# Performance work log

Hardware: AMD Instinct MI355X
Metric: run time of the kernel (lower is better)

The kernel has to match this reference:

```python
import jax, jax.numpy as jnp
import numpy as np

N, E, C_IN, C_OUT = 50000, 800000, 64, 64
BN_EPS = 1e-5


def _batchnorm(h, gamma, beta):
    # Training-mode BatchNorm1d: batch statistics over dim 0, biased variance.
    mean = h.mean(axis=0)
    var = h.var(axis=0)  # ddof=0, matches PyTorch normalization stats
    return gamma * (h - mean) * jax.lax.rsqrt(var + BN_EPS) + beta


def setup_inputs() -> dict:
    key = jax.random.key(0)
    ks = jax.random.split(key, 6)
    x = jax.random.normal(ks[0], (N, C_IN), dtype=jnp.float32)
    edge_index = jax.random.randint(ks[1], (2, E), 0, N, dtype=jnp.int32)
    edge_weight = jax.random.uniform(ks[2], (E,), dtype=jnp.float32)
    s1 = 1.0 / np.sqrt(C_IN).astype(np.float32)
    s2 = 1.0 / np.sqrt(2 * C_IN).astype(np.float32)
    pool_W = jax.random.uniform(ks[3], (C_IN, C_IN), jnp.float32, -s1, s1)
    pool_b = jnp.zeros((C_IN,), jnp.float32)
    final_W = jax.random.uniform(ks[4], (2 * C_IN, C_OUT), jnp.float32, -s2, s2)
    final_b = jnp.zeros((C_OUT,), jnp.float32)
    return {
        "x": x,
        "edge_index": edge_index,
        "edge_weight": edge_weight,
        "pool_W": pool_W,
        "pool_b": pool_b,
        "bn_pool_gamma": jnp.ones((C_IN,), jnp.float32),
        "bn_pool_beta": jnp.zeros((C_IN,), jnp.float32),
        "final_W": final_W,
        "final_b": final_b,
        "bn_final_gamma": jnp.ones((C_OUT,), jnp.float32),
        "bn_final_beta": jnp.zeros((C_OUT,), jnp.float32),
        "coef": jnp.float32(0.5),
    }


def reference(x, edge_index, edge_weight, pool_W, pool_b, bn_pool_gamma,
              bn_pool_beta, final_W, final_b, bn_final_gamma, bn_final_beta,
              coef):
    src, dst = edge_index[0], edge_index[1]
    # gather src node features, scale by edge weight  -> [E, C_IN]
    edge_feat = x[src] * (1.0 + coef * edge_weight[:, None])
    pooled = edge_feat @ pool_W + pool_b              # [E, C_IN]
    pooled = jax.nn.relu(_batchnorm(pooled, bn_pool_gamma, bn_pool_beta))
    # scatter-max into destination nodes; empty segments -> 0 (pooled >= 0)
    agg = jax.ops.segment_max(pooled, dst, num_segments=x.shape[0])
    agg = jnp.maximum(agg, 0.0)                       # fill -inf (empty) with 0
    h = jnp.concatenate([x, agg], axis=-1) @ final_W + final_b  # [N, C_OUT]
    h = _batchnorm(h, bn_final_gamma, bn_final_beta)
    return jax.nn.relu(h)
```

## Files before the change

### kernel.cpp

```cpp
#include <hip/hip_runtime.h>
#include <hip/hip_fp16.h>
#include <math.h>
#include <float.h>

#define BN_EPS 1e-5f
#define SLOTS 64


typedef __attribute__((ext_vector_type(8))) short bf16x8;
typedef __attribute__((ext_vector_type(4))) float f32x4;

__device__ inline unsigned short f2bf(float f) {
    unsigned u = __float_as_uint(f);
    return (unsigned short)((u + 0x7fffu + ((u >> 16) & 1u)) >> 16);
}
__device__ inline float bf2f(unsigned short h) {
    return __uint_as_float(((unsigned)h) << 16);
}

__global__ __launch_bounds__(256, 4) void k_scatter_pool(
        const int* __restrict__ src, const int* __restrict__ dst,
        const float* __restrict__ w, const float* __restrict__ coef_p,
        int* __restrict__ cnt, unsigned* __restrict__ csr, int E,
        const float* __restrict__ x, const float* __restrict__ W,
        unsigned short* __restrict__ ybf, int nrows, int SB) {
    __shared__ unsigned short Wt[64 * 72];
    if ((int)blockIdx.x < SB) {
        const float coef = *coef_p;
        for (int i = blockIdx.x * 256 + threadIdx.x; i < E; i += SB * 256) {
            int tn = dst[i];
            int sn = src[i];
            float s = fmaf(coef, w[i], 1.0f);
            unsigned hs = (unsigned)__half_as_ushort(__float2half(s));
            int pos = atomicAdd(&cnt[tn], 1);
            if (pos < SLOTS)
                csr[(size_t)tn * SLOTS + pos] = ((unsigned)sn << 16) | hs;
        }
        return;
    }
    for (int i = threadIdx.x; i < 64 * 64; i += 256) {
        int k = i >> 6, n = i & 63;
        Wt[n * 72 + k] = f2bf(W[i]);
    }
    __syncthreads();
    const int lane = threadIdx.x & 63;
    const int wave = threadIdx.x >> 6;
    const int quad = lane >> 4;
    const int ln = lane & 15;
    bf16x8 Bf[2][4];
#pragma unroll
    for (int kc = 0; kc < 2; ++kc)
#pragma unroll
        for (int ct = 0; ct < 4; ++ct)
            Bf[kc][ct] = *(const bf16x8*)&Wt[(ct * 16 + ln) * 72 + kc * 32 + quad * 8];
    const int T = (nrows + 15) >> 4;
    const int gw = ((int)blockIdx.x - SB) * 4 + wave;
    const int nw = ((int)gridDim.x - SB) * 4;
    for (int t = gw; t < T; t += nw) {
        const int row = t * 16 + ln;
        bf16x8 af[2];
        if (row < nrows) {
            const float* xr = x + (size_t)row * 64;
#pragma unroll
            for (int kc = 0; kc < 2; ++kc) {
                float4 pv = *(const float4*)(xr + kc * 32 + quad * 8);
                float4 qv = *(const float4*)(xr + kc * 32 + quad * 8 + 4);
                bf16x8 a;
                a[0] = (short)f2bf(pv.x); a[1] = (short)f2bf(pv.y);
                a[2] = (short)f2bf(pv.z); a[3] = (short)f2bf(pv.w);
                a[4] = (short)f2bf(qv.x); a[5] = (short)f2bf(qv.y);
                a[6] = (short)f2bf(qv.z); a[7] = (short)f2bf(qv.w);
                af[kc] = a;
            }
        } else {
            bf16x8 z;
#pragma unroll
            for (int j = 0; j < 8; ++j) z[j] = 0;
            af[0] = z; af[1] = z;
        }
        f32x4 acc[4];
#pragma unroll
        for (int ct = 0; ct < 4; ++ct) { acc[ct][0]=0.f; acc[ct][1]=0.f; acc[ct][2]=0.f; acc[ct][3]=0.f; }
#pragma unroll
        for (int ct = 0; ct < 4; ++ct) {
            acc[ct] = __builtin_amdgcn_mfma_f32_16x16x32_bf16(af[0], Bf[0][ct], acc[ct], 0, 0, 0);
            acc[ct] = __builtin_amdgcn_mfma_f32_16x16x32_bf16(af[1], Bf[1][ct], acc[ct], 0, 0, 0);
        }
#pragma unroll
        for (int r = 0; r < 4; ++r) {
            int ro = t * 16 + quad * 4 + r;
            if (ro < nrows) {
#pragma unroll
                for (int ct = 0; ct < 4; ++ct)
                    ybf[(size_t)ro * 64 + ct * 16 + ln] = f2bf(acc[ct][r]);
            }
        }
    }
}

__global__ __launch_bounds__(256) void k_gather_max(const unsigned short* __restrict__ ybf,
                             const unsigned* __restrict__ csr, const int* __restrict__ cnt,
                             float* __restrict__ M, float* __restrict__ pG2, int nrows) {
    int sub = threadIdx.x & 15;
    int rg = threadIdx.x >> 4;
    int c0 = sub * 4;
    float s1[4] = {0, 0, 0, 0}, s2[4] = {0, 0, 0, 0};
    const int nchunks = (nrows + 15) >> 4;
    for (int nb = blockIdx.x; nb < nchunks; nb += gridDim.x) {
        int node = nb * 16 + rg;
        size_t base = (size_t)node * SLOTS;
        int dg = 0;
        if (node < nrows) { dg = cnt[node]; if (dg > SLOTS) dg = SLOTS; }
        float m0 = -FLT_MAX, m1 = -FLT_MAX, m2 = -FLT_MAX, m3 = -FLT_MAX;
        for (int k0 = 0; k0 < dg; k0 += 16) {
            int kk = k0 + sub;
            unsigned pk = (kk < dg) ? csr[base + kk] : 0u;
            int cnt16 = dg - k0; if (cnt16 > 16) cnt16 = 16;
            for (int j = 0; j < cnt16; ++j) {
                unsigned r = (unsigned)__shfl((int)pk, j, 16);
                int sn = r >> 16;
                float sv = __half2float(__ushort_as_half((unsigned short)(r & 0xffffu)));
                ushort4 uv = *(const ushort4*)&ybf[(size_t)sn * 64 + c0];
                float v0 = sv * bf2f(uv.x), v1 = sv * bf2f(uv.y);
                float v2 = sv * bf2f(uv.z), v3 = sv * bf2f(uv.w);
                m0 = fmaxf(m0, v0); s1[0] += v0; s2[0] = fmaf(v0, v0, s2[0]);
                m1 = fmaxf(m1, v1); s1[1] += v1; s2[1] = fmaf(v1, v1, s2[1]);
                m2 = fmaxf(m2, v2); s1[2] += v2; s2[2] = fmaf(v2, v2, s2[2]);
                m3 = fmaxf(m3, v3); s1[3] += v3; s2[3] = fmaf(v3, v3, s2[3]);
            }
        }
        if (node < nrows)
            *(float4*)&M[(size_t)node * 64 + c0] = make_float4(m0, m1, m2, m3);
    }
    __shared__ float red[16][68];
    float* prow = pG2 + (size_t)(blockIdx.x & 127) * 128;
#pragma unroll
    for (int j = 0; j < 4; ++j) red[rg][c0 + j] = s1[j];
    __syncthreads();
    if (rg == 0) {
#pragma unroll
        for (int j = 0; j < 4; ++j) {
            float tt = 0.0f;
            for (int r = 0; r < 16; ++r) tt += red[r][c0 + j];
            atomicAdd(&prow[c0 + j], tt);
        }
    }
    __syncthreads();
#pragma unroll
    for (int j = 0; j < 4; ++j) red[rg][c0 + j] = s2[j];
    __syncthreads();
    if (rg == 0) {
#pragma unroll
        for (int j = 0; j < 4; ++j) {
            float tt = 0.0f;
            for (int r = 0; r < 16; ++r) tt += red[r][c0 + j];
            atomicAdd(&prow[64 + c0 + j], tt);
        }
    }
}

__global__ __launch_bounds__(1024) void k_red2(const float* __restrict__ p2,
                             const float* __restrict__ pool_b, const float* __restrict__ gamma,
                             const float* __restrict__ beta, float invE,
                             float* __restrict__ coef) {
    int c = threadIdx.x & 127;
    int seg = threadIdx.x >> 7;
    float acc = 0.0f;
    for (int r = seg; r < 128; r += 8) acc += p2[(size_t)r * 128 + c];
    __shared__ float red[8][128];
    red[seg][c] = acc;
    __syncthreads();
    if (seg == 0) {
        float tt = 0.0f;
#pragma unroll
        for (int s = 0; s < 8; ++s) tt += red[s][c];
        red[0][c] = tt;
    }
    __syncthreads();
    if (threadIdx.x < 64) {
        int c0 = threadIdx.x;
        float S1 = red[0][c0], S2 = red[0][64 + c0];
        float s1 = S1 * invE;
        float b = pool_b[c0];
        float mean = s1 + b;
        float ex2 = S2 * invE + 2.0f * b * s1 + b * b;
        float var = ex2 - mean * mean;
        float a = gamma[c0] * rsqrtf(var + BN_EPS);
        coef[c0] = a;
        coef[64 + c0] = beta[c0] - a * s1;
    }
}

__global__ __launch_bounds__(1024) void k_red2f(const float* __restrict__ p2,
                             const float* __restrict__ gamma, const float* __restrict__ beta,
                             float invN, float* __restrict__ coef) {
    int c = threadIdx.x & 127;
    int seg = threadIdx.x >> 7;
    float acc = 0.0f;
    for (int r = seg; r < 128; r += 8) acc += p2[(size_t)r * 128 + c];
    __shared__ float red[8][128];
    red[seg][c] = acc;
    __syncthreads();
    if (seg == 0) {
        float tt = 0.0f;
#pragma unroll
        for (int s = 0; s < 8; ++s) tt += red[s][c];
        red[0][c] = tt;
    }
    __syncthreads();
    if (threadIdx.x < 64) {
        int c0 = threadIdx.x;
        float mean = red[0][c0] * invN;
        float var = red[0][64 + c0] * invN - mean * mean;
        float a = gamma[c0] * rsqrtf(var + BN_EPS);
        coef[c0] = a;
        coef[64 + c0] = beta[c0] - a * mean;
    }
}

__global__ __launch_bounds__(256, 2) void k_final_gemm(const float* __restrict__ x,
                             const float* __restrict__ M, const float* __restrict__ coef,
                             const float* __restrict__ W, const float* __restrict__ b,
                             float* __restrict__ h, float* __restrict__ pF2, int nrows) {
    __shared__ unsigned short Wt[64 * 136];
    __shared__ float hp[128];
    for (int i = threadIdx.x; i < 128 * 64; i += 256) {
        int k = i >> 6, n = i & 63;
        Wt[n * 136 + k] = f2bf(W[i]);
    }
    if (threadIdx.x < 128) hp[threadIdx.x] = 0.0f;
    __syncthreads();
    const int lane = threadIdx.x & 63;
    const int wave = threadIdx.x >> 6;
    const int quad = lane >> 4;
    const int ln = lane & 15;
    bf16x8 Bf[4][4];
#pragma unroll
    for (int kc = 0; kc < 4; ++kc)
#pragma unroll
        for (int ct = 0; ct < 4; ++ct)
            Bf[kc][ct] = *(const bf16x8*)&Wt[(ct * 16 + ln) * 136 + kc * 32 + quad * 8];
    float bias[4];
#pragma unroll
    for (int ct = 0; ct < 4; ++ct) bias[ct] = b[ct * 16 + ln];
    float ca[2][8], cd[2][8];
#pragma unroll
    for (int g = 0; g < 2; ++g) {
        int ch = g * 32 + quad * 8;
#pragma unroll
        for (int j = 0; j < 8; ++j) {
            ca[g][j] = coef[ch + j];
            cd[g][j] = coef[64 + ch + j];
        }
    }
    float ls1[4] = {0, 0, 0, 0}, ls2[4] = {0, 0, 0, 0};
    const int T = (nrows + 15) >> 4;
    const int gw = blockIdx.x * 4 + wave;
    const int nw = gridDim.x * 4;
    for (int t = gw; t < T; t += nw) {
        const int row = t * 16 + ln;
        bf16x8 af[4];
        if (row < nrows) {
            const float* xr = x + (size_t)row * 64;
#pragma unroll
            for (int kc = 0; kc < 2; ++kc) {
                float4 pv = *(const float4*)(xr + kc * 32 + quad * 8);
                float4 qv = *(const float4*)(xr + kc * 32 + quad * 8 + 4);
                bf16x8 a;
                a[0] = (short)f2bf(pv.x); a[1] = (short)f2bf(pv.y);
                a[2] = (short)f2bf(pv.z); a[3] = (short)f2bf(pv.w);
                a[4] = (short)f2bf(qv.x); a[5] = (short)f2bf(qv.y);
                a[6] = (short)f2bf(qv.z); a[7] = (short)f2bf(qv.w);
                af[kc] = a;
            }
            const float* mr = M + (size_t)row * 64;
#pragma unroll
            for (int g = 0; g < 2; ++g) {
                const float* mp = mr + g * 32 + quad * 8;
                float4 pv = *(const float4*)mp;
                float4 qv = *(const float4*)(mp + 4);
                float v[8] = {pv.x, pv.y, pv.z, pv.w, qv.x, qv.y, qv.z, qv.w};
                bf16x8 a;
#pragma unroll
                for (int j = 0; j < 8; ++j)
                    a[j] = (short)f2bf(fmaxf(fmaf(ca[g][j], v[j], cd[g][j]), 0.0f));
                af[2 + g] = a;
            }
        } else {
            bf16x8 z;
#pragma unroll
            for (int j = 0; j < 8; ++j) z[j] = 0;
#pragma unroll
            for (int kc = 0; kc < 4; ++kc) af[kc] = z;
        }
        f32x4 acc[4];
#pragma unroll
        for (int ct = 0; ct < 4; ++ct) { acc[ct][0]=0.f; acc[ct][1]=0.f; acc[ct][2]=0.f; acc[ct][3]=0.f; }
#pragma unroll
        for (int kc = 0; kc < 4; ++kc)
#pragma unroll
            for (int ct = 0; ct < 4; ++ct)
                acc[ct] = __builtin_amdgcn_mfma_f32_16x16x32_bf16(af[kc], Bf[kc][ct], acc[ct], 0, 0, 0);
#pragma unroll
        for (int r = 0; r < 4; ++r) {
            int ro = t * 16 + quad * 4 + r;
            if (ro < nrows) {
#pragma unroll
                for (int ct = 0; ct < 4; ++ct) {
                    float hv = acc[ct][r] + bias[ct];
                    h[(size_t)ro * 64 + ct * 16 + ln] = hv;
                    ls1[ct] += hv;
                    ls2[ct] = fmaf(hv, hv, ls2[ct]);
                }
            }
        }
    }
#pragma unroll
    for (int ct = 0; ct < 4; ++ct) {
        atomicAdd(&hp[ct * 16 + ln], ls1[ct]);
        atomicAdd(&hp[64 + ct * 16 + ln], ls2[ct]);
    }
    __syncthreads();
    if (threadIdx.x < 128)
        atomicAdd(&pF2[(size_t)(blockIdx.x & 127) * 128 + threadIdx.x], hp[threadIdx.x]);
}

__global__ __launch_bounds__(256) void k_bn_out(const float* __restrict__ h,
                         const float* __restrict__ coef,
                         float* __restrict__ out, int nrows) {
    const int idx = blockIdx.x * blockDim.x + threadIdx.x;
    const int total = nrows * 16;
    if (idx >= total) return;
    const int c0 = (idx & 15) * 4;
    const float4 hv = *(const float4*)(h + (size_t)idx * 4);
    float4 o;
    float* op = (float*)&o;
    const float* hp = (const float*)&hv;
#pragma unroll
    for (int j = 0; j < 4; ++j) {
        const int c = c0 + j;
        op[j] = fmaxf(fmaf(coef[c], hp[j], coef[64 + c]), 0.0f);
    }
    *(float4*)(out + (size_t)idx * 4) = o;
}

extern "C" void kernel_launch(void* const* d_in, const int* in_sizes, int n_in,
                              void* d_out, int out_size, void* d_ws, size_t ws_size,
                              hipStream_t stream) {
    const float* x       = (const float*)d_in[0];
    const int*   eidx    = (const int*)d_in[1];
    const float* ew      = (const float*)d_in[2];
    const float* pool_W  = (const float*)d_in[3];
    const float* pool_b  = (const float*)d_in[4];
    const float* g1      = (const float*)d_in[5];
    const float* b1      = (const float*)d_in[6];
    const float* final_W = (const float*)d_in[7];
    const float* final_b = (const float*)d_in[8];
    const float* g2      = (const float*)d_in[9];
    const float* b2      = (const float*)d_in[10];
    const float* coef    = (const float*)d_in[11];

    const int N = in_sizes[0] / 64;
    const int E = in_sizes[1] / 2;
    const int* src = eidx;
    const int* dst = eidx + E;

    const int SB  = 3072;
    const int T   = (N + 15) / 16;
    const int nbT = (T + 3) / 4;
    const int PG  = 1024;

    unsigned* ws = (unsigned*)d_ws;
    int*   cnt    = (int*)ws;
    float* pG2    = (float*)(ws + (size_t)N);
    float* pF2    = (float*)(ws + (size_t)N + 16384);
    float* bncoef = (float*)(ws + (size_t)N + 32768);
    float* coef2  = (float*)(ws + (size_t)N + 32896);
    unsigned short* ybf = (unsigned short*)(ws + (size_t)N + 33024);
    unsigned* csr = ws + (size_t)N + 33024 + (size_t)32 * N;
    float* M      = (float*)(csr + (size_t)SLOTS * N);

    hipMemsetAsync(d_ws, 0, ((size_t)N + 32768) * 4, stream);

    k_scatter_pool<<<SB + nbT, 256, 0, stream>>>(src, dst, ew, coef, cnt, csr, E,
                                                 x, pool_W, ybf, N, SB);
    k_gather_max<<<PG, 256, 0, stream>>>(ybf, csr, cnt, M, pG2, N);
    k_red2   <<<1, 1024, 0, stream>>>(pG2, pool_b, g1, b1, 1.0f / (float)E, bncoef);
    k_final_gemm<<<nbT, 256, 0, stream>>>(x, M, bncoef, final_W, final_b,
                                          (float*)d_out, pF2, N);
    k_red2f  <<<1, 1024, 0, stream>>>(pF2, g2, b2, 1.0f / (float)N, coef2);
    k_bn_out <<<(N * 16 + 255) / 256, 256, 0, stream>>>((const float*)d_out, coef2,
                                                        (float*)d_out, N);
}
```

Measured before the change: 221.9 us.

## Merge pipeline into one cooperative persistent kernel with grid barriers

Replaces the six separate launches (scatter+pool GEMM, gather-max, two BN reductions, final GEMM, BN output) with one persistent cooperative kernel that runs four phases separated by atomic grid barriers. The single-block BN statistic reductions are folded into the start of the next phase, with every block redundantly recomputing the coefficients. This removes launch gaps and tiny serial kernels. In exchange the grid is capped by occupancy (at most 1024 blocks), each phase uses fewer blocks than before, and the spin barriers plus host occupancy and device-property queries on every call add overhead.

```diff
diff --git a/kernel.cpp b/kernel.cpp
--- a/kernel.cpp
+++ b/kernel.cpp
@@ -18,330 +18,318 @@
     return __uint_as_float(((unsigned)h) << 16);
 }
 
-__global__ __launch_bounds__(256, 4) void k_scatter_pool(
+__device__ __forceinline__ void grid_bar(int* bcnt, int bar_idx) {
+    __syncthreads();
+    if (threadIdx.x == 0) {
+        __threadfence();
+        __hip_atomic_fetch_add(bcnt, 1, __ATOMIC_RELEASE, __HIP_MEMORY_SCOPE_AGENT);
+        const int target = (int)gridDim.x * bar_idx;
+        while (__hip_atomic_load(bcnt, __ATOMIC_RELAXED, __HIP_MEMORY_SCOPE_AGENT) < target)
+            __builtin_amdgcn_s_sleep(2);
+        __threadfence();
+    }
+    __syncthreads();
+}
+
+__global__ __launch_bounds__(256, 4) void k_mega(
         const int* __restrict__ src, const int* __restrict__ dst,
         const float* __restrict__ w, const float* __restrict__ coef_p,
-        int* __restrict__ cnt, unsigned* __restrict__ csr, int E,
-        const float* __restrict__ x, const float* __restrict__ W,
-        unsigned short* __restrict__ ybf, int nrows, int SB) {
-    __shared__ unsigned short Wt[64 * 72];
-    if ((int)blockIdx.x < SB) {
-        const float coef = *coef_p;
-        for (int i = blockIdx.x * 256 + threadIdx.x; i < E; i += SB * 256) {
-            int tn = dst[i];
-            int sn = src[i];
-            float s = fmaf(coef, w[i], 1.0f);
-            unsigned hs = (unsigned)__half_as_ushort(__float2half(s));
-            int pos = atomicAdd(&cnt[tn], 1);
-            if (pos < SLOTS)
-                csr[(size_t)tn * SLOTS + pos] = ((unsigned)sn << 16) | hs;
+        const float* __restrict__ x,
+        const float* __restrict__ pool_W, const float* __restrict__ pool_b,
+        const float* __restrict__ g1, const float* __restrict__ b1,
+        const float* __restrict__ final_W, const float* __restrict__ final_b,
+        const float* __restrict__ g2, const float* __restrict__ b2,
+        int* bcnt, int* __restrict__ cnt, unsigned* __restrict__ csr,
+        unsigned short* __restrict__ ybf, float* __restrict__ M,
+        float* __restrict__ pG2, float* __restrict__ pF2,
+        float* __restrict__ h, int N, int E, int SCB, int plo, int phi) {
+    __shared__ unsigned short Wt[64 * 136];
+    __shared__ float redf[16][68];
+    __shared__ float bnc[128];
+    __shared__ float hp[128];
+    const int tid = threadIdx.x;
+    const int bid = blockIdx.x;
+    const int nb  = gridDim.x;
+    const int lane = tid & 63;
+    const int wave = tid >> 6;
+    const int quad = lane >> 4;
+    const int ln   = lane & 15;
+    float* redflat = (float*)redf;
+
+    for (int ph = plo; ph <= phi; ++ph) {
+        switch (ph) {
+        case 0: {
+            if (bid < SCB) {
+                const float coef = *coef_p;
+                for (int i = bid * 256 + tid; i < E; i += SCB * 256) {
+                    int tn = dst[i];
+                    int sn = src[i];
+                    float s = fmaf(coef, w[i], 1.0f);
+                    unsigned hs = (unsigned)__half_as_ushort(__float2half(s));
+                    int pos = atomicAdd(&cnt[tn], 1);
+                    if (pos < SLOTS)
+                        csr[(size_t)tn * SLOTS + pos] = ((unsigned)sn << 16) | hs;
+                }
+            } else {
+                for (int i = tid; i < 64 * 64; i += 256) {
+                    int k = i >> 6, n = i & 63;
+                    Wt[n * 72 + k] = f2bf(pool_W[i]);
+                }
+                __syncthreads();
+                bf16x8 Bf[2][4];
+#pragma unroll
+                for (int kc = 0; kc < 2; ++kc)
+#pragma unroll
+                    for (int ct = 0; ct < 4; ++ct)
+                        Bf[kc][ct] = *(const bf16x8*)&Wt[(ct * 16 + ln) * 72 + kc * 32 + quad * 8];
+                const int T = (N + 15) >> 4;
+                const int gw = (bid - SCB) * 4 + wave;
+                const int nw = (nb - SCB) * 4;
+                for (int t = gw; t < T; t += nw) {
+                    const int row = t * 16 + ln;
+                    bf16x8 af[2];
+                    if (row < N) {
+                        const float* xr = x + (size_t)row * 64;
+#pragma unroll
+                        for (int kc = 0; kc < 2; ++kc) {
+                            float4 pv = *(const float4*)(xr + kc * 32 + quad * 8);
+                            float4 qv = *(const float4*)(xr + kc * 32 + quad * 8 + 4);
+                            bf16x8 a;
+                            a[0] = (short)f2bf(pv.x); a[1] = (short)f2bf(pv.y);
+                            a[2] = (short)f2bf(pv.z); a[3] = (short)f2bf(pv.w);
+                            a[4] = (short)f2bf(qv.x); a[5] = (short)f2bf(qv.y);
+                            a[6] = (short)f2bf(qv.z); a[7] = (short)f2bf(qv.w);
+                            af[kc] = a;
+                        }
+                    } else {
+                        bf16x8 z;
+#pragma unroll
+                        for (int j = 0; j < 8; ++j) z[j] = 0;
+                        af[0] = z; af[1] = z;
+                    }
+                    f32x4 acc[4];
+#pragma unroll
+                    for (int ct = 0; ct < 4; ++ct) { acc[ct][0]=0.f; acc[ct][1]=0.f; acc[ct][2]=0.f; acc[ct][3]=0.f; }
+#pragma unroll
+                    for (int ct = 0; ct < 4; ++ct) {
+                        acc[ct] = __builtin_amdgcn_mfma_f32_16x16x32_bf16(af[0], Bf[0][ct], acc[ct], 0, 0, 0);
+                        acc[ct] = __builtin_amdgcn_mfma_f32_16x16x32_bf16(af[1], Bf[1][ct], acc[ct], 0, 0, 0);
+                    }
+#pragma unroll
+                    for (int r = 0; r < 4; ++r) {
+                        int ro = t * 16 + quad * 4 + r;
+                        if (ro < N) {
+#pragma unroll
+                            for (int ct = 0; ct < 4; ++ct)
+                                ybf[(size_t)ro * 64 + ct * 16 + ln] = f2bf(acc[ct][r]);
+                        }
+                    }
+                }
+            }
+            break;
         }
-        return;
+        case 1: {
+            int sub = tid & 15;
+            int rg = tid >> 4;
+            int c0 = sub * 4;
+            float s1[4] = {0, 0, 0, 0}, s2[4] = {0, 0, 0, 0};
+            const int nchunks = (N + 15) >> 4;
+            for (int nbk = bid; nbk < nchunks; nbk += nb) {
+                int node = nbk * 16 + rg;
+                size_t base = (size_t)node * SLOTS;
+                int dg = 0;
+                if (node < N) { dg = cnt[node]; if (dg > SLOTS) dg = SLOTS; }
+                float m0 = -FLT_MAX, m1 = -FLT_MAX, m2 = -FLT_MAX, m3 = -FLT_MAX;
+                for (int k0 = 0; k0 < dg; k0 += 16) {
+                    int kk = k0 + sub;
+                    unsigned pk = (kk < dg) ? csr[base + kk] : 0u;
+                    int cnt16 = dg - k0; if (cnt16 > 16) cnt16 = 16;
+                    for (int j = 0; j < cnt16; ++j) {
+                        unsigned r = (unsigned)__shfl((int)pk, j, 16);
+                        int sn = r >> 16;
+                        float sv = __half2float(__ushort_as_half((unsigned short)(r & 0xffffu)));
+                        ushort4 uv = *(const ushort4*)&ybf[(size_t)sn * 64 + c0];
+                        float v0 = sv * bf2f(uv.x), v1 = sv * bf2f(uv.y);
+                        float v2 = sv * bf2f(uv.z), v3 = sv * bf2f(uv.w);
+                        m0 = fmaxf(m0, v0); s1[0] += v0; s2[0] = fmaf(v0, v0, s2[0]);
+                        m1 = fmaxf(m1, v1); s1[1] += v1; s2[1] = fmaf(v1, v1, s2[1]);
+                        m2 = fmaxf(m2, v2); s1[2] += v2; s2[2] = fmaf(v2, v2, s2[2]);
+                        m3 = fmaxf(m3, v3); s1[3] += v3; s2[3] = fmaf(v3, v3, s2[3]);
+                    }
+                }
+                if (node < N)
+                    *(float4*)&M[(size_t)node * 64 + c0] = make_float4(m0, m1, m2, m3);
+            }
+            float* prow = pG2 + (size_t)(bid & 127) * 128;
+            __syncthreads();
+#pragma unroll
+            for (int j = 0; j < 4; ++j) redf[rg][c0 + j] = s1[j];
+            __syncthreads();
+            if (rg == 0) {
+#pragma unroll
+                for (int j = 0; j < 4; ++j) {
+                    float tt = 0.0f;
+                    for (int r = 0; r < 16; ++r) tt += redf[r][c0 + j];
+                    atomicAdd(&prow[c0 + j], tt);
+                }
+            }
+            __syncthreads();
+#pragma unroll
+            for (int j = 0; j < 4; ++j) redf[rg][c0 + j] = s2[j];
+            __syncthreads();
+            if (rg == 0) {
+#pragma unroll
+                for (int j = 0; j < 4; ++j) {
+                    float tt = 0.0f;
+                    for (int r = 0; r < 16; ++r) tt += redf[r][c0 + j];
+                    atomicAdd(&prow[64 + c0 + j], tt);
+                }
+            }
+            break;
+        }
+        case 2: {
+            for (int i = tid; i < 128 * 64; i += 256) {
+                int k = i >> 6, n = i & 63;
+                Wt[n * 136 + k] = f2bf(final_W[i]);
+            }
+            int c = tid & 127, seg = tid >> 7;
+            float acc = 0.0f;
+            for (int r = seg; r < 128; r += 2) acc += pG2[(size_t)r * 128 + c];
+            __syncthreads();
+            redflat[tid] = acc;
+            __syncthreads();
+            if (tid < 64) {
+                float S1 = redflat[tid] + redflat[128 + tid];
+                float S2 = redflat[64 + tid] + redflat[192 + tid];
+                float invE = 1.0f / (float)E;
+                float s1m = S1 * invE;
+                float bb = pool_b[tid];
+                float mean = s1m + bb;
+                float ex2 = S2 * invE + 2.0f * bb * s1m + bb * bb;
+                float var = ex2 - mean * mean;
+                float a = g1[tid] * rsqrtf(var + BN_EPS);
+                bnc[tid] = a;
+                bnc[64 + tid] = b1[tid] - a * s1m;
+            }
+            if (tid < 128) hp[tid] = 0.0f;
+            __syncthreads();
+
+            bf16x8 Bf[4][4];
+#pragma unroll
+            for (int kc = 0; kc < 4; ++kc)
+#pragma unroll
+                for (int ct = 0; ct < 4; ++ct)
+                    Bf[kc][ct] = *(const bf16x8*)&Wt[(ct * 16 + ln) * 136 + kc * 32 + quad * 8];
+            float bias[4];
+#pragma unroll
+            for (int ct = 0; ct < 4; ++ct) bias[ct] = final_b[ct * 16 + ln];
+            float ls1[4] = {0, 0, 0, 0}, ls2[4] = {0, 0, 0, 0};
+            const int T = (N + 15) >> 4;
+            const int gw = bid * 4 + wave;
+            const int nw = nb * 4;
+            for (int t = gw; t < T; t += nw) {
+                const int row = t * 16 + ln;
+                bf16x8 af[4];
+                if (row < N) {
+                    const float* xr = x + (size_t)row * 64;
+#pragma unroll
+                    for (int kc = 0; kc < 2; ++kc) {
+                        float4 pv = *(const float4*)(xr + kc * 32 + quad * 8);
+                        float4 qv = *(const float4*)(xr + kc * 32 + quad * 8 + 4);
+                        bf16x8 a;
+                        a[0] = (short)f2bf(pv.x); a[1] = (short)f2bf(pv.y);
+                        a[2] = (short)f2bf(pv.z); a[3] = (short)f2bf(pv.w);
+                        a[4] = (short)f2bf(qv.x); a[5] = (short)f2bf(qv.y);
+                        a[6] = (short)f2bf(qv.z); a[7] = (short)f2bf(qv.w);
+                        af[kc] = a;
+                    }
+                    const float* mr = M + (size_t)row * 64;
+#pragma unroll
+                    for (int g = 0; g < 2; ++g) {
+                        const float* mp = mr + g * 32 + quad * 8;
+                        float4 pv = *(const float4*)mp;
+                        float4 qv = *(const float4*)(mp + 4);
+                        float v[8] = {pv.x, pv.y, pv.z, pv.w, qv.x, qv.y, qv.z, qv.w};
+                        int ch = g * 32 + quad * 8;
+                        bf16x8 a;
+#pragma unroll
+                        for (int j = 0; j < 8; ++j)
+                            a[j] = (short)f2bf(fmaxf(fmaf(bnc[ch + j], v[j], bnc[64 + ch + j]), 0.0f));
+                        af[2 + g] = a;
+                    }
+                } else {
+                    bf16x8 z;
+#pragma unroll
+                    for (int j = 0; j < 8; ++j) z[j] = 0;
+#pragma unroll
+                    for (int kc = 0; kc < 4; ++kc) af[kc] = z;
+                }
+                f32x4 acc4[4];
+#pragma unroll
+                for (int ct = 0; ct < 4; ++ct) { acc4[ct][0]=0.f; acc4[ct][1]=0.f; acc4[ct][2]=0.f; acc4[ct][3]=0.f; }
+#pragma unroll
+                for (int kc = 0; kc < 4; ++kc)
+#pragma unroll
+                    for (int ct = 0; ct < 4; ++ct)
+                        acc4[ct] = __builtin_amdgcn_mfma_f32_16x16x32_bf16(af[kc], Bf[kc][ct], acc4[ct], 0, 0, 0);
+#pragma unroll
+                for (int r = 0; r < 4; ++r) {
+                    int ro = t * 16 + quad * 4 + r;
+                    if (ro < N) {
+#pragma unroll
+                        for (int ct = 0; ct < 4; ++ct) {
+                            float hv = acc4[ct][r] + bias[ct];
+                            h[(size_t)ro * 64 + ct * 16 + ln] = hv;
+                            ls1[ct] += hv;
+                            ls2[ct] = fmaf(hv, hv, ls2[ct]);
+                        }
+                    }
+                }
+            }
+#pragma unroll
+            for (int ct = 0; ct < 4; ++ct) {
+                atomicAdd(&hp[ct * 16 + ln], ls1[ct]);
+                atomicAdd(&hp[64 + ct * 16 + ln], ls2[ct]);
+            }
+            __syncthreads();
+            if (tid < 128)
+                atomicAdd(&pF2[(size_t)(bid & 127) * 128 + tid], hp[tid]);
+            break;
+        }
+        case 3: {
+            int c = tid & 127, seg = tid >> 7;
+            float acc = 0.0f;
+            for (int r = seg; r < 128; r += 2) acc += pF2[(size_t)r * 128 + c];
+            __syncthreads();
+            redflat[tid] = acc;
+            __syncthreads();
+            if (tid < 64) {
+                float S1 = redflat[tid] + redflat[128 + tid];
+                float S2 = redflat[64 + tid] + redflat[192 + tid];
+                float invN = 1.0f / (float)N;
+                float mean = S1 * invN;
+                float var = S2 * invN - mean * mean;
+                float a = g2[tid] * rsqrtf(var + BN_EPS);
+                bnc[tid] = a;
+                bnc[64 + tid] = b2[tid] - a * mean;
+            }
+            __syncthreads();
+            const int total = N * 16;
+            for (int idx = bid * 256 + tid; idx < total; idx += nb * 256) {
+                const int c0 = (idx & 15) * 4;
+                float4 hv = *(const float4*)(h + (size_t)idx * 4);
+                float4 o;
+                o.x = fmaxf(fmaf(bnc[c0 + 0], hv.x, bnc[64 + c0 + 0]), 0.0f);
+                o.y = fmaxf(fmaf(bnc[c0 + 1], hv.y, bnc[64 + c0 + 1]), 0.0f);
+                o.z = fmaxf(fmaf(bnc[c0 + 2], hv.z, bnc[64 + c0 + 2]), 0.0f);
+                o.w = fmaxf(fmaf(bnc[c0 + 3], hv.w, bnc[64 + c0 + 3]), 0.0f);
+                *(float4*)(h + (size_t)idx * 4) = o;
+            }
+            break;
+        }
+        }
+        if (ph < phi) grid_bar(bcnt, ph - plo + 1);
     }
-    for (int i = threadIdx.x; i < 64 * 64; i += 256) {
-        int k = i >> 6, n = i & 63;
-        Wt[n * 72 + k] = f2bf(W[i]);
-    }
-    __syncthreads();
-    const int lane = threadIdx.x & 63;
-    const int wave = threadIdx.x >> 6;
-    const int quad = lane >> 4;
-    const int ln = lane & 15;
-    bf16x8 Bf[2][4];
-#pragma unroll
-    for (int kc = 0; kc < 2; ++kc)
-#pragma unroll
-        for (int ct = 0; ct < 4; ++ct)
-            Bf[kc][ct] = *(const bf16x8*)&Wt[(ct * 16 + ln) * 72 + kc * 32 + quad * 8];
-    const int T = (nrows + 15) >> 4;
-    const int gw = ((int)blockIdx.x - SB) * 4 + wave;
-    const int nw = ((int)gridDim.x - SB) * 4;
-    for (int t = gw; t < T; t += nw) {
-        const int row = t * 16 + ln;
-        bf16x8 af[2];
-        if (row < nrows) {
-            const float* xr = x + (size_t)row * 64;
-#pragma unroll
-            for (int kc = 0; kc < 2; ++kc) {
-                float4 pv = *(const float4*)(xr + kc * 32 + quad * 8);
-                float4 qv = *(const float4*)(xr + kc * 32 + quad * 8 + 4);
-                bf16x8 a;
-                a[0] = (short)f2bf(pv.x); a[1] = (short)f2bf(pv.y);
-                a[2] = (short)f2bf(pv.z); a[3] = (short)f2bf(pv.w);
-                a[4] = (short)f2bf(qv.x); a[5] = (short)f2bf(qv.y);
-                a[6] = (short)f2bf(qv.z); a[7] = (short)f2bf(qv.w);
-                af[kc] = a;
-            }
-        } else {
-            bf16x8 z;
-#pragma unroll
-            for (int j = 0; j < 8; ++j) z[j] = 0;
-            af[0] = z; af[1] = z;
-        }
-        f32x4 acc[4];
-#pragma unroll
-        for (int ct = 0; ct < 4; ++ct) { acc[ct][0]=0.f; acc[ct][1]=0.f; acc[ct][2]=0.f; acc[ct][3]=0.f; }
-#pragma unroll
-        for (int ct = 0; ct < 4; ++ct) {
-            acc[ct] = __builtin_amdgcn_mfma_f32_16x16x32_bf16(af[0], Bf[0][ct], acc[ct], 0, 0, 0);
-            acc[ct] = __builtin_amdgcn_mfma_f32_16x16x32_bf16(af[1], Bf[1][ct], acc[ct], 0, 0, 0);
-        }
-#pragma unroll
-        for (int r = 0; r < 4; ++r) {
-            int ro = t * 16 + quad * 4 + r;
-            if (ro < nrows) {
-#pragma unroll
-                for (int ct = 0; ct < 4; ++ct)
-                    ybf[(size_t)ro * 64 + ct * 16 + ln] = f2bf(acc[ct][r]);
-            }
-        }
-    }
-}
-
-__global__ __launch_bounds__(256) void k_gather_max(const unsigned short* __restrict__ ybf,
-                             const unsigned* __restrict__ csr, const int* __restrict__ cnt,
-                             float* __restrict__ M, float* __restrict__ pG2, int nrows) {
-    int sub = threadIdx.x & 15;
-    int rg = threadIdx.x >> 4;
-    int c0 = sub * 4;
-    float s1[4] = {0, 0, 0, 0}, s2[4] = {0, 0, 0, 0};
-    const int nchunks = (nrows + 15) >> 4;
-    for (int nb = blockIdx.x; nb < nchunks; nb += gridDim.x) {
-        int node = nb * 16 + rg;
-        size_t base = (size_t)node * SLOTS;
-        int dg = 0;
-        if (node < nrows) { dg = cnt[node]; if (dg > SLOTS) dg = SLOTS; }
-        float m0 = -FLT_MAX, m1 = -FLT_MAX, m2 = -FLT_MAX, m3 = -FLT_MAX;
-        for (int k0 = 0; k0 < dg; k0 += 16) {
-            int kk = k0 + sub;
-            unsigned pk = (kk < dg) ? csr[base + kk] : 0u;
-            int cnt16 = dg - k0; if (cnt16 > 16) cnt16 = 16;
-            for (int j = 0; j < cnt16; ++j) {
-                unsigned r = (unsigned)__shfl((int)pk, j, 16);
-                int sn = r >> 16;
-                float sv = __half2float(__ushort_as_half((unsigned short)(r & 0xffffu)));
-                ushort4 uv = *(const ushort4*)&ybf[(size_t)sn * 64 + c0];
-                float v0 = sv * bf2f(uv.x), v1 = sv * bf2f(uv.y);
-                float v2 = sv * bf2f(uv.z), v3 = sv * bf2f(uv.w);
-                m0 = fmaxf(m0, v0); s1[0] += v0; s2[0] = fmaf(v0, v0, s2[0]);
-                m1 = fmaxf(m1, v1); s1[1] += v1; s2[1] = fmaf(v1, v1, s2[1]);
-                m2 = fmaxf(m2, v2); s1[2] += v2; s2[2] = fmaf(v2, v2, s2[2]);
-                m3 = fmaxf(m3, v3); s1[3] += v3; s2[3] = fmaf(v3, v3, s2[3]);
-            }
-        }
-        if (node < nrows)
-            *(float4*)&M[(size_t)node * 64 + c0] = make_float4(m0, m1, m2, m3);
-    }
-    __shared__ float red[16][68];
-    float* prow = pG2 + (size_t)(blockIdx.x & 127) * 128;
-#pragma unroll
-    for (int j = 0; j < 4; ++j) red[rg][c0 + j] = s1[j];
-    __syncthreads();
-    if (rg == 0) {
-#pragma unroll
-        for (int j = 0; j < 4; ++j) {
-            float tt = 0.0f;
-            for (int r = 0; r < 16; ++r) tt += red[r][c0 + j];
-            atomicAdd(&prow[c0 + j], tt);
-        }
-    }
-    __syncthreads();
-#pragma unroll
-    for (int j = 0; j < 4; ++j) red[rg][c0 + j] = s2[j];
-    __syncthreads();
-    if (rg == 0) {
-#pragma unroll
-        for (int j = 0; j < 4; ++j) {
-            float tt = 0.0f;
-            for (int r = 0; r < 16; ++r) tt += red[r][c0 + j];
-            atomicAdd(&prow[64 + c0 + j], tt);
-        }
-    }
-}
-
-__global__ __launch_bounds__(1024) void k_red2(const float* __restrict__ p2,
-                             const float* __restrict__ pool_b, const float* __restrict__ gamma,
-                             const float* __restrict__ beta, float invE,
-                             float* __restrict__ coef) {
-    int c = threadIdx.x & 127;
-    int seg = threadIdx.x >> 7;
-    float acc = 0.0f;
-    for (int r = seg; r < 128; r += 8) acc += p2[(size_t)r * 128 + c];
-    __shared__ float red[8][128];
-    red[seg][c] = acc;
-    __syncthreads();
-    if (seg == 0) {
-        float tt = 0.0f;
-#pragma unroll
-        for (int s = 0; s < 8; ++s) tt += red[s][c];
-        red[0][c] = tt;
-    }
-    __syncthreads();
-    if (threadIdx.x < 64) {
-        int c0 = threadIdx.x;
-        float S1 = red[0][c0], S2 = red[0][64 + c0];
-        float s1 = S1 * invE;
-        float b = pool_b[c0];
-        float mean = s1 + b;
-        float ex2 = S2 * invE + 2.0f * b * s1 + b * b;
-        float var = ex2 - mean * mean;
-        float a = gamma[c0] * rsqrtf(var + BN_EPS);
-        coef[c0] = a;
-        coef[64 + c0] = beta[c0] - a * s1;
-    }
-}
-
-__global__ __launch_bounds__(1024) void k_red2f(const float* __restrict__ p2,
-                             const float* __restrict__ gamma, const float* __restrict__ beta,
-                             float invN, float* __restrict__ coef) {
-    int c = threadIdx.x & 127;
-    int seg = threadIdx.x >> 7;
-    float acc = 0.0f;
-    for (int r = seg; r < 128; r += 8) acc += p2[(size_t)r * 128 + c];
-    __shared__ float red[8][128];
-    red[seg][c] = acc;
-    __syncthreads();
-    if (seg == 0) {
-        float tt = 0.0f;
-#pragma unroll
-        for (int s = 0; s < 8; ++s) tt += red[s][c];
-        red[0][c] = tt;
-    }
-    __syncthreads();
-    if (threadIdx.x < 64) {
-        int c0 = threadIdx.x;
-        float mean = red[0][c0] * invN;
-        float var = red[0][64 + c0] * invN - mean * mean;
-        float a = gamma[c0] * rsqrtf(var + BN_EPS);
-        coef[c0] = a;
-        coef[64 + c0] = beta[c0] - a * mean;
-    }
-}
-
-__global__ __launch_bounds__(256, 2) void k_final_gemm(const float* __restrict__ x,
-                             const float* __restrict__ M, const float* __restrict__ coef,
-                             const float* __restrict__ W, const float* __restrict__ b,
-                             float* __restrict__ h, float* __restrict__ pF2, int nrows) {
-    __shared__ unsigned short Wt[64 * 136];
-    __shared__ float hp[128];
-    for (int i = threadIdx.x; i < 128 * 64; i += 256) {
-        int k = i >> 6, n = i & 63;
-        Wt[n * 136 + k] = f2bf(W[i]);
-    }
-    if (threadIdx.x < 128) hp[threadIdx.x] = 0.0f;
-    __syncthreads();
-    const int lane = threadIdx.x & 63;
-    const int wave = threadIdx.x >> 6;
-    const int quad = lane >> 4;
-    const int ln = lane & 15;
-    bf16x8 Bf[4][4];
-#pragma unroll
-    for (int kc = 0; kc < 4; ++kc)
-#pragma unroll
-        for (int ct = 0; ct < 4; ++ct)
-            Bf[kc][ct] = *(const bf16x8*)&Wt[(ct * 16 + ln) * 136 + kc * 32 + quad * 8];
-    float bias[4];
-#pragma unroll
-    for (int ct = 0; ct < 4; ++ct) bias[ct] = b[ct * 16 + ln];
-    float ca[2][8], cd[2][8];
-#pragma unroll
-    for (int g = 0; g < 2; ++g) {
-        int ch = g * 32 + quad * 8;
-#pragma unroll
-        for (int j = 0; j < 8; ++j) {
-            ca[g][j] = coef[ch + j];
-            cd[g][j] = coef[64 + ch + j];
-        }
-    }
-    float ls1[4] = {0, 0, 0, 0}, ls2[4] = {0, 0, 0, 0};
-    const int T = (nrows + 15) >> 4;
-    const int gw = blockIdx.x * 4 + wave;
-    const int nw = gridDim.x * 4;
-    for (int t = gw; t < T; t += nw) {
-        const int row = t * 16 + ln;
-        bf16x8 af[4];
-        if (row < nrows) {
-            const float* xr = x + (size_t)row * 64;
-#pragma unroll
-            for (int kc = 0; kc < 2; ++kc) {
-                float4 pv = *(const float4*)(xr + kc * 32 + quad * 8);
-                float4 qv = *(const float4*)(xr + kc * 32 + quad * 8 + 4);
-                bf16x8 a;
-                a[0] = (short)f2bf(pv.x); a[1] = (short)f2bf(pv.y);
-                a[2] = (short)f2bf(pv.z); a[3] = (short)f2bf(pv.w);
-                a[4] = (short)f2bf(qv.x); a[5] = (short)f2bf(qv.y);
-                a[6] = (short)f2bf(qv.z); a[7] = (short)f2bf(qv.w);
-                af[kc] = a;
-            }
-            const float* mr = M + (size_t)row * 64;
-#pragma unroll
-            for (int g = 0; g < 2; ++g) {
-                const float* mp = mr + g * 32 + quad * 8;
-                float4 pv = *(const float4*)mp;
-                float4 qv = *(const float4*)(mp + 4);
-                float v[8] = {pv.x, pv.y, pv.z, pv.w, qv.x, qv.y, qv.z, qv.w};
-                bf16x8 a;
-#pragma unroll
-                for (int j = 0; j < 8; ++j)
-                    a[j] = (short)f2bf(fmaxf(fmaf(ca[g][j], v[j], cd[g][j]), 0.0f));
-                af[2 + g] = a;
-            }
-        } else {
-            bf16x8 z;
-#pragma unroll
-            for (int j = 0; j < 8; ++j) z[j] = 0;
-#pragma unroll
-            for (int kc = 0; kc < 4; ++kc) af[kc] = z;
-        }
-        f32x4 acc[4];
-#pragma unroll
-        for (int ct = 0; ct < 4; ++ct) { acc[ct][0]=0.f; acc[ct][1]=0.f; acc[ct][2]=0.f; acc[ct][3]=0.f; }
-#pragma unroll
-        for (int kc = 0; kc < 4; ++kc)
-#pragma unroll
-            for (int ct = 0; ct < 4; ++ct)
-                acc[ct] = __builtin_amdgcn_mfma_f32_16x16x32_bf16(af[kc], Bf[kc][ct], acc[ct], 0, 0, 0);
-#pragma unroll
-        for (int r = 0; r < 4; ++r) {
-            int ro = t * 16 + quad * 4 + r;
-            if (ro < nrows) {
-#pragma unroll
-                for (int ct = 0; ct < 4; ++ct) {
-                    float hv = acc[ct][r] + bias[ct];
-                    h[(size_t)ro * 64 + ct * 16 + ln] = hv;
-                    ls1[ct] += hv;
-                    ls2[ct] = fmaf(hv, hv, ls2[ct]);
-                }
-            }
-        }
-    }
-#pragma unroll
-    for (int ct = 0; ct < 4; ++ct) {
-        atomicAdd(&hp[ct * 16 + ln], ls1[ct]);
-        atomicAdd(&hp[64 + ct * 16 + ln], ls2[ct]);
-    }
-    __syncthreads();
-    if (threadIdx.x < 128)
-        atomicAdd(&pF2[(size_t)(blockIdx.x & 127) * 128 + threadIdx.x], hp[threadIdx.x]);
-}
-
-__global__ __launch_bounds__(256) void k_bn_out(const float* __restrict__ h,
-                         const float* __restrict__ coef,
-                         float* __restrict__ out, int nrows) {
-    const int idx = blockIdx.x * blockDim.x + threadIdx.x;
-    const int total = nrows * 16;
-    if (idx >= total) return;
-    const int c0 = (idx & 15) * 4;
-    const float4 hv = *(const float4*)(h + (size_t)idx * 4);
-    float4 o;
-    float* op = (float*)&o;
-    const float* hp = (const float*)&hv;
-#pragma unroll
-    for (int j = 0; j < 4; ++j) {
-        const int c = c0 + j;
-        op[j] = fmaxf(fmaf(coef[c], hp[j], coef[64 + c]), 0.0f);
-    }
-    *(float4*)(out + (size_t)idx * 4) = o;
 }
 
 extern "C" void kernel_launch(void* const* d_in, const int* in_sizes, int n_in,
@@ -360,35 +348,69 @@
     const float* b2      = (const float*)d_in[10];
     const float* coef    = (const float*)d_in[11];
 
-    const int N = in_sizes[0] / 64;
-    const int E = in_sizes[1] / 2;
+    int N = in_sizes[0] / 64;
+    int E = in_sizes[1] / 2;
     const int* src = eidx;
     const int* dst = eidx + E;
 
-    const int SB  = 3072;
-    const int T   = (N + 15) / 16;
-    const int nbT = (T + 3) / 4;
-    const int PG  = 1024;
-
     unsigned* ws = (unsigned*)d_ws;
-    int*   cnt    = (int*)ws;
-    float* pG2    = (float*)(ws + (size_t)N);
-    float* pF2    = (float*)(ws + (size_t)N + 16384);
-    float* bncoef = (float*)(ws + (size_t)N + 32768);
-    float* coef2  = (float*)(ws + (size_t)N + 32896);
-    unsigned short* ybf = (unsigned short*)(ws + (size_t)N + 33024);
-    unsigned* csr = ws + (size_t)N + 33024 + (size_t)32 * N;
+    int*   bcnt  = (int*)ws;
+    int*   cnt   = (int*)(ws + 2);
+    float* pG2   = (float*)(ws + 2 + (size_t)N);
+    float* pF2   = (float*)(ws + 2 + (size_t)N + 16384);
+    unsigned short* ybf = (unsigned short*)(ws + 2 + (size_t)N + 32768);
+    unsigned* csr = ws + 2 + (size_t)N + 32768 + (size_t)32 * N;
     float* M      = (float*)(csr + (size_t)SLOTS * N);
-
-    hipMemsetAsync(d_ws, 0, ((size_t)N + 32768) * 4, stream);
-
-    k_scatter_pool<<<SB + nbT, 256, 0, stream>>>(src, dst, ew, coef, cnt, csr, E,
-                                                 x, pool_W, ybf, N, SB);
-    k_gather_max<<<PG, 256, 0, stream>>>(ybf, csr, cnt, M, pG2, N);
-    k_red2   <<<1, 1024, 0, stream>>>(pG2, pool_b, g1, b1, 1.0f / (float)E, bncoef);
-    k_final_gemm<<<nbT, 256, 0, stream>>>(x, M, bncoef, final_W, final_b,
-                                          (float*)d_out, pF2, N);
-    k_red2f  <<<1, 1024, 0, stream>>>(pF2, g2, b2, 1.0f / (float)N, coef2);
-    k_bn_out <<<(N * 16 + 255) / 256, 256, 0, stream>>>((const float*)d_out, coef2,
-                                                        (float*)d_out, N);
+    float* h      = (float*)d_out;
+
+    hipMemsetAsync(d_ws, 0, ((size_t)N + 32770) * 4, stream);
+
+    int maxPerCU = 0;
+    hipOccupancyMaxActiveBlocksPerMultiprocessor(&maxPerCU, k_mega, 256, 0);
+    if (maxPerCU < 1) maxPerCU = 1;
+    hipDeviceProp_t prop;
+    int dev = 0;
+    hipGetDevice(&dev);
+    hipGetDeviceProperties(&prop, dev);
+    int grid = prop.multiProcessorCount * maxPerCU;
+    if (grid > 1024) grid = 1024;
+    if (grid < 16) grid = 16;
+    int SCB = (grid * 3) / 4;
+    int plo = 0, phi = 3;
+
+    const int*   a_src = src;      const int*   a_dst = dst;
+    const float* a_w = ew;         const float* a_coef = coef;
+    const float* a_x = x;
+    const float* a_pW = pool_W;    const float* a_pb = pool_b;
+    const float* a_g1 = g1;        const float* a_b1 = b1;
+    const float* a_fW = final_W;   const float* a_fb = final_b;
+    const float* a_g2 = g2;        const float* a_b2 = b2;
+    void* kargs[] = {
+        (void*)&a_src, (void*)&a_dst, (void*)&a_w, (void*)&a_coef, (void*)&a_x,
+        (void*)&a_pW, (void*)&a_pb, (void*)&a_g1, (void*)&a_b1,
+        (void*)&a_fW, (void*)&a_fb, (void*)&a_g2, (void*)&a_b2,
+        (void*)&bcnt, (void*)&cnt, (void*)&csr, (void*)&ybf, (void*)&M,
+        (void*)&pG2, (void*)&pF2, (void*)&h,
+        (void*)&N, (void*)&E, (void*)&SCB, (void*)&plo, (void*)&phi };
+
+    hipError_t err = hipLaunchCooperativeKernel((void*)k_mega, dim3(grid),
+                                                dim3(256), kargs, 0, stream);
+    if (err != hipSuccess) {
+        k_mega<<<grid, 256, 0, stream>>>(src, dst, ew, coef, x, pool_W, pool_b,
+                                         g1, b1, final_W, final_b, g2, b2,
+                                         bcnt, cnt, csr, ybf, M, pG2, pF2,
+                                         h, N, E, SCB, 0, 0);
+        k_mega<<<grid, 256, 0, stream>>>(src, dst, ew, coef, x, pool_W, pool_b,
+                                         g1, b1, final_W, final_b, g2, b2,
+                                         bcnt, cnt, csr, ybf, M, pG2, pF2,
+                                         h, N, E, SCB, 1, 1);
+        k_mega<<<grid, 256, 0, stream>>>(src, dst, ew, coef, x, pool_W, pool_b,
+                                         g1, b1, final_W, final_b, g2, b2,
+                                         bcnt, cnt, csr, ybf, M, pG2, pF2,
+                                         h, N, E, SCB, 2, 2);
+        k_mega<<<grid, 256, 0, stream>>>(src, dst, ew, coef, x, pool_W, pool_b,
+                                         g1, b1, final_W, final_b, g2, b2,
+                                         bcnt, cnt, csr, ybf, M, pG2, pF2,
+                                         h, N, E, SCB, 3, 3);
+    }
 }
```

New measurement: 489.1 us. 120% more time.
